# Kernel tuning notes

Hardware: AMD Instinct MI355X
Metric: run time of the kernel (lower is better)

The kernel has to match this reference:

```python
import jax, jax.numpy as jnp
import numpy as np

B = 4096      # batch_size from init_kwargs
D = 128       # projection embedding dim
TAU = 0.5     # temperature
EPS = 1e-8    # torch CosineSimilarity eps


def _neg_indices(n):
    # Static column indices of the 2n-2 negatives per row (diagonal and the
    # +/-n positive pair are excluded), matching the boolean-mask reshape.
    mask = np.ones((2 * n, 2 * n), dtype=bool)
    np.fill_diagonal(mask, False)
    idx = np.arange(n)
    mask[idx, idx + n] = False
    mask[idx + n, idx] = False
    return jnp.asarray(np.nonzero(mask)[1].reshape(2 * n, 2 * n - 2))

_NEG_IDX = _neg_indices(B)


def setup_inputs() -> dict:
    key = jax.random.key(0)
    k1, k2 = jax.random.split(key)
    return {
        "z_i": jax.random.normal(k1, (B, D), dtype=jnp.float32),
        "z_j": jax.random.normal(k2, (B, D), dtype=jnp.float32),
    }


def reference(z_i, z_j):
    n = B
    p = jnp.concatenate([z_i, z_j], axis=0)                      # [2N, D]
    norm = jnp.linalg.norm(p, axis=1, keepdims=True)
    pn = p / jnp.maximum(norm, EPS)                              # cosine normalize
    sim = jnp.matmul(pn, pn.T) / TAU                             # [2N, 2N]
    pos = jnp.concatenate([jnp.diagonal(sim, n), jnp.diagonal(sim, -n)])[:, None]  # [2N,1]
    neg = jnp.take_along_axis(sim, _NEG_IDX, axis=1)             # [2N, 2N-2]
    logits = jnp.concatenate([pos, neg], axis=1)                 # [2N, 2N-1], label = 0
    # CrossEntropyLoss(reduction='sum') with label 0, divided by 2N
    loss = jnp.sum(jax.nn.logsumexp(logits, axis=1) - logits[:, 0]) / (2 * n)
    return loss
```

## Files before the change

### kernel.cpp

```cpp
#include <hip/hip_runtime.h>
#include <cmath>

#define DIM 128
#define NHALF 4096
#define NROWS 8192
#define NB 128
#define NTILES 8256
#define FRAG_SCALE 1.69864368f

typedef __attribute__((ext_vector_type(8))) short bf16x8;
typedef __attribute__((ext_vector_type(4))) float f32x4;

static __device__ __forceinline__ unsigned short f32_to_bf16(float f) {
  unsigned int u = __float_as_uint(f);
  u = (u + 0x7FFFu + ((u >> 16) & 1u)) >> 16;
  return (unsigned short)u;
}

template <int CTRL>
static __device__ __forceinline__ float dpp_radd(float v) {
  int t = __builtin_amdgcn_update_dpp(0, __float_as_int(v), CTRL, 0xF, 0xF,
                                      false);
  return v + __int_as_float(t);
}
static __device__ __forceinline__ float row16_allreduce(float v) {
  v = dpp_radd<0x121>(v);
  v = dpp_radd<0x122>(v);
  v = dpp_radd<0x124>(v);
  v = dpp_radd<0x128>(v);
  return v;
}


__global__ __launch_bounds__(256) void prep_kernel(
    const float* __restrict__ z_i, const float* __restrict__ z_j,
    unsigned int* __restrict__ A, float* __restrict__ pos,
    float* __restrict__ out) {
  int wave = threadIdx.x >> 6;
  int lane = threadIdx.x & 63;
  int r = blockIdx.x * 4 + wave;
  if (blockIdx.x == 0 && threadIdx.x == 0) out[0] = 0.0f;
  float2 a = *(const float2*)(z_i + (size_t)r * DIM + 2 * lane);
  float2 b = *(const float2*)(z_j + (size_t)r * DIM + 2 * lane);
  float sa = a.x * a.x + a.y * a.y;
  float sb = b.x * b.x + b.y * b.y;
  float dp = a.x * b.x + a.y * b.y;
#pragma unroll
  for (int off = 1; off < 64; off <<= 1) {
    sa += __shfl_xor(sa, off);
    sb += __shfl_xor(sb, off);
    dp += __shfl_xor(dp, off);
  }
  float na = fmaxf(sqrtf(sa), 1e-8f);
  float nb = fmaxf(sqrtf(sb), 1e-8f);
  float si = FRAG_SCALE / na;
  float sj = FRAG_SCALE / nb;
  unsigned int pa = (unsigned int)f32_to_bf16(a.x * si) |
                    ((unsigned int)f32_to_bf16(a.y * si) << 16);
  unsigned int pb = (unsigned int)f32_to_bf16(b.x * sj) |
                    ((unsigned int)f32_to_bf16(b.y * sj) << 16);
  int rg = r >> 4;
  int n = r & 15;
  int kc = lane >> 4;
  int q = (lane >> 2) & 3;
  int bq = lane & 3;
  int off4 = rg * 1024 + kc * 256 + q * 64 + n * 4 + bq;
  A[off4] = pa;
  A[off4 + 262144] = pb;
  if (lane == 0) {
    float p = dp / (na * nb) * 2.0f;
    pos[r] = p;
    pos[r + NHALF] = p;
  }
}

__global__ __launch_bounds__(256, 4) void simexp_kernel(
    const unsigned int* __restrict__ Au, float* __restrict__ partials) {
  const int lane = threadIdx.x & 63;
  const int w = threadIdx.x >> 6;
  const int q = lane >> 4;
  const int n = lane & 15;

  int g = blockIdx.x * 4 + w;
  int ti = (int)((257.0f - sqrtf(66049.0f - 8.0f * (float)g)) * 0.5f);
  int start = 128 * ti - (ti * (ti - 1)) / 2;
  if (g < start) {
    ti--;
    start = 128 * ti - (ti * (ti - 1)) / 2;
  } else if (g >= start + (128 - ti)) {
    start += 128 - ti;
    ti++;
  }
  int tj = ti + (g - start);
  const bool diag = (ti == tj);

  const bf16x8* frag = (const bf16x8*)Au + lane;

  f32x4 acc[16];
#pragma unroll
  for (int i = 0; i < 16; i++)
#pragma unroll
    for (int j = 0; j < 4; j++) acc[i][j] = 0.0f;

#pragma unroll
  for (int kc = 0; kc < 4; kc++) {
    bf16x8 af[4], bfr[4];
#pragma unroll
    for (int mi = 0; mi < 4; mi++)
      af[mi] = frag[(size_t)(ti * 16 + mi * 4 + kc) * 64];
#pragma unroll
    for (int ni = 0; ni < 4; ni++)
      bfr[ni] = frag[(size_t)(tj * 16 + ni * 4 + kc) * 64];
#pragma unroll
    for (int mi = 0; mi < 4; mi++)
#pragma unroll
      for (int ni = 0; ni < 4; ni++)
        acc[mi * 4 + ni] = __builtin_amdgcn_mfma_f32_16x16x32_bf16(
            af[mi], bfr[ni], acc[mi * 4 + ni], 0, 0, 0);
  }

  float eaccR[16];
  float eaccC[4];
#pragma unroll
  for (int i = 0; i < 16; i++) eaccR[i] = 0.0f;
#pragma unroll
  for (int i = 0; i < 4; i++) eaccC[i] = 0.0f;
  if (diag) {
#pragma unroll
    for (int mi = 0; mi < 4; mi++)
#pragma unroll
      for (int ni = 0; ni < 4; ni++)
#pragma unroll
        for (int rg = 0; rg < 4; rg++) {
          float e = __builtin_amdgcn_exp2f(acc[mi * 4 + ni][rg]);
          e = ((mi * 16 + q * 4 + rg) == (ni * 16 + n)) ? 0.0f : e;
          eaccR[mi * 4 + rg] += e;
          eaccC[ni] += e;
        }
  } else {
#pragma unroll
    for (int mi = 0; mi < 4; mi++)
#pragma unroll
      for (int ni = 0; ni < 4; ni++)
#pragma unroll
        for (int rg = 0; rg < 4; rg++) {
          float e = __builtin_amdgcn_exp2f(acc[mi * 4 + ni][rg]);
          eaccR[mi * 4 + rg] += e;
          eaccC[ni] += e;
        }
  }

  const int dslot = tj - ti;
  float* prow = partials + (size_t)dslot * NROWS + ti * 64;
#pragma unroll
  for (int mi = 0; mi < 4; mi++) {
#pragma unroll
    for (int rg = 0; rg < 4; rg++) {
      float v = row16_allreduce(eaccR[mi * 4 + rg]);
      if (n == 0) prow[mi * 16 + q * 4 + rg] = v;
    }
  }
  if (!diag) {
    float* pcol = partials + (size_t)(128 - dslot) * NROWS + tj * 64;
#pragma unroll
    for (int ni = 0; ni < 4; ni++) {
      float v = eaccC[ni];
      v += __shfl_xor(v, 16);
      v += __shfl_xor(v, 32);
      if (lane < 16) pcol[ni * 16 + lane] = v;
    }
  }
}

__global__ __launch_bounds__(256) void finalize_kernel(
    const float* __restrict__ partials, const float* __restrict__ pos,
    float* __restrict__ out) {
  int tid = threadIdx.x;
  int rr = tid & 31;
  int ks = tid >> 5;
  int r = blockIdx.x * 32 + rr;
  float s = 0.0f;
#pragma unroll
  for (int k = 0; k < 16; k++)
    s += partials[(size_t)(ks * 16 + k) * NROWS + r];
  __shared__ float red[8][32];
  red[ks][rr] = s;
  __syncthreads();
  if (tid < 32) {
    float t = 0.0f;
#pragma unroll
    for (int k2 = 0; k2 < 8; k2++) t += red[k2][tid];
    float local = logf(t) - pos[blockIdx.x * 32 + tid];
#pragma unroll
    for (int off = 1; off < 32; off <<= 1) local += __shfl_xor(local, off);
    if (tid == 0) atomicAdd(out, local * (1.0f / (float)NROWS));
  }
}

extern "C" void kernel_launch(void* const* d_in, const int* in_sizes, int n_in,
                              void* d_out, int out_size, void* d_ws,
                              size_t ws_size, hipStream_t stream) {
  const float* z_i = (const float*)d_in[0];
  const float* z_j = (const float*)d_in[1];
  float* out = (float*)d_out;

  unsigned int* A = (unsigned int*)d_ws;
  float* partials = (float*)((char*)d_ws + (1u << 21));
  float* pos = (float*)((char*)d_ws + (3u << 21));

  prep_kernel<<<NHALF / 4, 256, 0, stream>>>(z_i, z_j, A, pos, out);
  simexp_kernel<<<NTILES / 4, 256, 0, stream>>>((const unsigned int*)A,
                                                partials);
  finalize_kernel<<<NROWS / 32, 256, 0, stream>>>(partials, pos, out);
}
```

Before: 81.32 us.

## Fuse prep, simexp and finalize into one cooperative persistent kernel

Merges the three launches into a single cooperative kernel that separates the stages with grid-wide syncs and walks each stage's work with grid-stride loops. The aim is to remove per-launch overhead and the idle gaps between kernels. The grid is capped at 1024 persistent blocks sized from an occupancy query, and the old three-kernel path remains as a fallback. The cost is two grid barriers, and with fewer blocks the triangular tile work may balance less well than one wave per tile.

```diff
diff --git a/kernel.cpp b/kernel.cpp
--- a/kernel.cpp
+++ b/kernel.cpp
@@ -1,10 +1,12 @@
 #include <hip/hip_runtime.h>
+#include <hip/hip_cooperative_groups.h>
 #include <cmath>
+
+namespace cg = cooperative_groups;
 
 #define DIM 128
 #define NHALF 4096
 #define NROWS 8192
-#define NB 128
 #define NTILES 8256
 #define FRAG_SCALE 1.69864368f
 
@@ -32,14 +34,11 @@
 }
 
 
-__global__ __launch_bounds__(256) void prep_kernel(
-    const float* __restrict__ z_i, const float* __restrict__ z_j,
-    unsigned int* __restrict__ A, float* __restrict__ pos,
-    float* __restrict__ out) {
-  int wave = threadIdx.x >> 6;
-  int lane = threadIdx.x & 63;
-  int r = blockIdx.x * 4 + wave;
-  if (blockIdx.x == 0 && threadIdx.x == 0) out[0] = 0.0f;
+
+static __device__ __forceinline__ void prep_body(
+    int r, int lane, const float* __restrict__ z_i,
+    const float* __restrict__ z_j, unsigned int* __restrict__ A,
+    float* __restrict__ pos) {
   float2 a = *(const float2*)(z_i + (size_t)r * DIM + 2 * lane);
   float2 b = *(const float2*)(z_j + (size_t)r * DIM + 2 * lane);
   float sa = a.x * a.x + a.y * a.y;
@@ -74,14 +73,12 @@
   }
 }
 
-__global__ __launch_bounds__(256, 4) void simexp_kernel(
-    const unsigned int* __restrict__ Au, float* __restrict__ partials) {
-  const int lane = threadIdx.x & 63;
-  const int w = threadIdx.x >> 6;
+static __device__ __forceinline__ void simexp_body(
+    int g, int lane, const unsigned int* __restrict__ Au,
+    float* __restrict__ partials) {
   const int q = lane >> 4;
   const int n = lane & 15;
 
-  int g = blockIdx.x * 4 + w;
   int ti = (int)((257.0f - sqrtf(66049.0f - 8.0f * (float)g)) * 0.5f);
   int start = 128 * ti - (ti * (ti - 1)) / 2;
   if (g < start) {
@@ -172,29 +169,84 @@
   }
 }
 
-__global__ __launch_bounds__(256) void finalize_kernel(
-    const float* __restrict__ partials, const float* __restrict__ pos,
-    float* __restrict__ out) {
-  int tid = threadIdx.x;
+static __device__ __forceinline__ void finalize_body(
+    int chunk, int tid, const float* __restrict__ partials,
+    const float* __restrict__ pos, float* __restrict__ out,
+    float red[8][32]) {
   int rr = tid & 31;
   int ks = tid >> 5;
-  int r = blockIdx.x * 32 + rr;
+  int r = chunk * 32 + rr;
   float s = 0.0f;
 #pragma unroll
   for (int k = 0; k < 16; k++)
     s += partials[(size_t)(ks * 16 + k) * NROWS + r];
-  __shared__ float red[8][32];
   red[ks][rr] = s;
   __syncthreads();
   if (tid < 32) {
     float t = 0.0f;
 #pragma unroll
     for (int k2 = 0; k2 < 8; k2++) t += red[k2][tid];
-    float local = logf(t) - pos[blockIdx.x * 32 + tid];
+    float local = logf(t) - pos[chunk * 32 + tid];
 #pragma unroll
     for (int off = 1; off < 32; off <<= 1) local += __shfl_xor(local, off);
     if (tid == 0) atomicAdd(out, local * (1.0f / (float)NROWS));
   }
+}
+
+__global__ __launch_bounds__(256, 4) void fused_kernel(
+    const float* __restrict__ z_i, const float* __restrict__ z_j,
+    unsigned int* __restrict__ A, float* __restrict__ partials,
+    float* __restrict__ pos, float* __restrict__ out) {
+  const int tid = threadIdx.x;
+  const int lane = tid & 63;
+  const int w = tid >> 6;
+  const int nwaves = gridDim.x << 2;
+  const int gw0 = (blockIdx.x << 2) + w;
+  __shared__ float red[8][32];
+
+  for (int r = gw0; r < NHALF; r += nwaves)
+    prep_body(r, lane, z_i, z_j, A, pos);
+  if (blockIdx.x == 0 && tid == 0) out[0] = 0.0f;
+
+  cg::grid_group grid = cg::this_grid();
+  __threadfence();
+  grid.sync();
+
+  for (int g = gw0; g < NTILES; g += nwaves) simexp_body(g, lane, A, partials);
+
+  __threadfence();
+  grid.sync();
+
+  for (int chunk = blockIdx.x; chunk < (NROWS / 32); chunk += gridDim.x) {
+    finalize_body(chunk, tid, partials, pos, out, red);
+    __syncthreads();
+  }
+}
+
+
+__global__ __launch_bounds__(256) void prep_kernel(
+    const float* __restrict__ z_i, const float* __restrict__ z_j,
+    unsigned int* __restrict__ A, float* __restrict__ pos,
+    float* __restrict__ out) {
+  int wave = threadIdx.x >> 6;
+  int lane = threadIdx.x & 63;
+  int r = blockIdx.x * 4 + wave;
+  if (blockIdx.x == 0 && threadIdx.x == 0) out[0] = 0.0f;
+  prep_body(r, lane, z_i, z_j, A, pos);
+}
+
+__global__ __launch_bounds__(256, 4) void simexp_kernel(
+    const unsigned int* __restrict__ Au, float* __restrict__ partials) {
+  const int lane = threadIdx.x & 63;
+  const int w = threadIdx.x >> 6;
+  simexp_body(blockIdx.x * 4 + w, lane, Au, partials);
+}
+
+__global__ __launch_bounds__(256) void finalize_kernel(
+    const float* __restrict__ partials, const float* __restrict__ pos,
+    float* __restrict__ out) {
+  __shared__ float red[8][32];
+  finalize_body(blockIdx.x, threadIdx.x, partials, pos, out, red);
 }
 
 extern "C" void kernel_launch(void* const* d_in, const int* in_sizes, int n_in,
@@ -208,8 +260,35 @@
   float* partials = (float*)((char*)d_ws + (1u << 21));
   float* pos = (float*)((char*)d_ws + (3u << 21));
 
-  prep_kernel<<<NHALF / 4, 256, 0, stream>>>(z_i, z_j, A, pos, out);
-  simexp_kernel<<<NTILES / 4, 256, 0, stream>>>((const unsigned int*)A,
-                                                partials);
-  finalize_kernel<<<NROWS / 32, 256, 0, stream>>>(partials, pos, out);
-}
+  static int coopBlocks = -1;
+  if (coopBlocks < 0) {
+    int perCU = 0;
+    if (hipOccupancyMaxActiveBlocksPerMultiprocessor(&perCU, fused_kernel,
+                                                     256, 0) == hipSuccess &&
+        perCU > 0) {
+      long nb = (long)perCU * 256;
+      coopBlocks = (int)(nb > 1024 ? 1024 : nb);
+    } else {
+      coopBlocks = 0;
+    }
+  }
+
+  bool launched = false;
+  if (coopBlocks > 0) {
+    void* args[] = {(void*)&z_i, (void*)&z_j, (void*)&A,
+                    (void*)&partials, (void*)&pos, (void*)&out};
+    hipError_t e = hipLaunchCooperativeKernel(
+        fused_kernel, dim3(coopBlocks), dim3(256), args, 0, stream);
+    if (e == hipSuccess) {
+      launched = true;
+    } else {
+      coopBlocks = 0;
+    }
+  }
+  if (!launched) {
+    prep_kernel<<<NHALF / 4, 256, 0, stream>>>(z_i, z_j, A, pos, out);
+    simexp_kernel<<<NTILES / 4, 256, 0, stream>>>((const unsigned int*)A,
+                                                  partials);
+    finalize_kernel<<<NROWS / 32, 256, 0, stream>>>(partials, pos, out);
+  }
+}
```

After: 296.0 us. 3.64x slower.

## Fuse finalize into simexp kernel via atomic completion counter

Applied to the files above, without the earlier changes.

Folds the finalize kernel into the simexp launch as 64 extra trailing blocks. These spin on a global atomic counter until all simexp blocks have finished and fenced their partials, then do the row reductions and log-sum. This removes one kernel launch and its inter-kernel gap. In exchange it adds a spin-wait that depends on the trailing blocks being scheduled after the others (true for in-order dispatch) and leaves 64 blocks occupying CU slots while they wait.

```diff
diff --git a/kernel.cpp b/kernel.cpp
--- a/kernel.cpp
+++ b/kernel.cpp
@@ -4,8 +4,9 @@
 #define DIM 128
 #define NHALF 4096
 #define NROWS 8192
-#define NB 128
 #define NTILES 8256
+#define NSIMEXP 2064
+#define NFINAL 64
 #define FRAG_SCALE 1.69864368f
 
 typedef __attribute__((ext_vector_type(8))) short bf16x8;
@@ -35,11 +36,14 @@
 __global__ __launch_bounds__(256) void prep_kernel(
     const float* __restrict__ z_i, const float* __restrict__ z_j,
     unsigned int* __restrict__ A, float* __restrict__ pos,
-    float* __restrict__ out) {
+    float* __restrict__ out, unsigned int* __restrict__ counter) {
   int wave = threadIdx.x >> 6;
   int lane = threadIdx.x & 63;
   int r = blockIdx.x * 4 + wave;
-  if (blockIdx.x == 0 && threadIdx.x == 0) out[0] = 0.0f;
+  if (blockIdx.x == 0 && threadIdx.x == 0) {
+    out[0] = 0.0f;
+    counter[0] = 0u;
+  }
   float2 a = *(const float2*)(z_i + (size_t)r * DIM + 2 * lane);
   float2 b = *(const float2*)(z_j + (size_t)r * DIM + 2 * lane);
   float sa = a.x * a.x + a.y * a.y;
@@ -74,14 +78,12 @@
   }
 }
 
-__global__ __launch_bounds__(256, 4) void simexp_kernel(
-    const unsigned int* __restrict__ Au, float* __restrict__ partials) {
-  const int lane = threadIdx.x & 63;
-  const int w = threadIdx.x >> 6;
+static __device__ __forceinline__ void simexp_body(
+    int g, int lane, const unsigned int* __restrict__ Au,
+    float* __restrict__ partials) {
   const int q = lane >> 4;
   const int n = lane & 15;
 
-  int g = blockIdx.x * 4 + w;
   int ti = (int)((257.0f - sqrtf(66049.0f - 8.0f * (float)g)) * 0.5f);
   int start = 128 * ti - (ti * (ti - 1)) / 2;
   if (g < start) {
@@ -172,29 +174,61 @@
   }
 }
 
-__global__ __launch_bounds__(256) void finalize_kernel(
-    const float* __restrict__ partials, const float* __restrict__ pos,
-    float* __restrict__ out) {
-  int tid = threadIdx.x;
+static __device__ __forceinline__ void finalize_body(
+    int chunk, int tid, const float* __restrict__ partials,
+    const float* __restrict__ pos, float* __restrict__ out,
+    float red[8][32]) {
   int rr = tid & 31;
   int ks = tid >> 5;
-  int r = blockIdx.x * 32 + rr;
+  int r = chunk * 32 + rr;
   float s = 0.0f;
 #pragma unroll
   for (int k = 0; k < 16; k++)
     s += partials[(size_t)(ks * 16 + k) * NROWS + r];
-  __shared__ float red[8][32];
   red[ks][rr] = s;
   __syncthreads();
   if (tid < 32) {
     float t = 0.0f;
 #pragma unroll
     for (int k2 = 0; k2 < 8; k2++) t += red[k2][tid];
-    float local = logf(t) - pos[blockIdx.x * 32 + tid];
+    float local = logf(t) - pos[chunk * 32 + tid];
 #pragma unroll
     for (int off = 1; off < 32; off <<= 1) local += __shfl_xor(local, off);
     if (tid == 0) atomicAdd(out, local * (1.0f / (float)NROWS));
   }
+}
+
+__global__ __launch_bounds__(256, 4) void simexp_kernel(
+    const unsigned int* __restrict__ Au, float* __restrict__ partials,
+    const float* __restrict__ pos, float* __restrict__ out,
+    unsigned int* __restrict__ counter) {
+  const int tid = threadIdx.x;
+  __shared__ float red[8][32];
+
+  if (blockIdx.x >= NSIMEXP) {
+    if (tid == 0) {
+      while (__hip_atomic_load(counter, __ATOMIC_ACQUIRE,
+                               __HIP_MEMORY_SCOPE_AGENT) < NSIMEXP)
+        __builtin_amdgcn_s_sleep(2);
+    }
+    __syncthreads();
+    __threadfence();
+    int fb = blockIdx.x - NSIMEXP;
+#pragma unroll
+    for (int i = 0; i < 4; i++) {
+      finalize_body(fb * 4 + i, tid, partials, pos, out, red);
+      __syncthreads();
+    }
+    return;
+  }
+
+  const int lane = tid & 63;
+  const int w = tid >> 6;
+  simexp_body(blockIdx.x * 4 + w, lane, Au, partials);
+
+  __threadfence();
+  __syncthreads();
+  if (tid == 0) atomicAdd(counter, 1u);
 }
 
 extern "C" void kernel_launch(void* const* d_in, const int* in_sizes, int n_in,
@@ -207,9 +241,10 @@
   unsigned int* A = (unsigned int*)d_ws;
   float* partials = (float*)((char*)d_ws + (1u << 21));
   float* pos = (float*)((char*)d_ws + (3u << 21));
-
-  prep_kernel<<<NHALF / 4, 256, 0, stream>>>(z_i, z_j, A, pos, out);
-  simexp_kernel<<<NTILES / 4, 256, 0, stream>>>((const unsigned int*)A,
-                                                partials);
-  finalize_kernel<<<NROWS / 32, 256, 0, stream>>>(partials, pos, out);
-}
+  unsigned int* counter =
+      (unsigned int*)((char*)d_ws + (3u << 21) + 32768);
+
+  prep_kernel<<<NHALF / 4, 256, 0, stream>>>(z_i, z_j, A, pos, out, counter);
+  simexp_kernel<<<NSIMEXP + NFINAL, 256, 0, stream>>>(
+      (const unsigned int*)A, partials, pos, out, counter);
+}
```

After: 276.2 us. 240% more time.
